# Performance work log

Measured on AMD Instinct MI355X. Metric: run time of the kernel, lower is better.

## Reference

```python
import jax, jax.numpy as jnp
import numpy as np

DIM = 1024
NUM_HEADS = 16
HEAD_DIM = DIM // NUM_HEADS
MLP_RATIO = 4
NUM_EXPERTS = 4
B, N = 4, 1024


def _ln(x, g, b, eps=1e-5):
    m = jnp.mean(x, axis=-1, keepdims=True)
    v = jnp.mean(jnp.square(x - m), axis=-1, keepdims=True)
    return (x - m) * jax.lax.rsqrt(v + eps) * g + b


def setup_inputs() -> dict:
    key = jax.random.key(0)
    ks = jax.random.split(key, 8)
    d = DIM
    return {
        "x": jax.random.normal(ks[0], (B, N, d), jnp.float32),
        "expert_mask": jax.random.randint(ks[1], (B, N), 0, NUM_EXPERTS),
        "expert_probs": jax.random.uniform(ks[2], (B, N, 1), jnp.float32),
        "expand_weight": 0.02 * jax.random.normal(ks[3], (3 * d + MLP_RATIO * d, d), jnp.float32),
        "mlp_bias": 0.02 * jax.random.normal(ks[4], (MLP_RATIO * d,), jnp.float32),
        "contract_weight": 0.02 * jax.random.normal(ks[5], (2 * d, d + MLP_RATIO * d), jnp.float32),
        "contract_bias": 0.02 * jax.random.normal(ks[6], (2 * d,), jnp.float32),
        "norm1_g": jnp.ones((d,), jnp.float32),
        "norm1_b": jnp.zeros((d,), jnp.float32),
        "norm2_g": jnp.ones((d,), jnp.float32),
        "norm2_b": jnp.zeros((d,), jnp.float32),
        "alpha": 0.1 * jax.random.normal(ks[7], (1,), jnp.float32),
    }


def reference(x, expert_mask, expert_probs, expand_weight, mlp_bias, contract_weight,
              contract_bias, norm1_g, norm1_b, norm2_g, norm2_b, alpha):
    Bx, Nx, D = x.shape
    # nested capacity per token: D_e = D // 2**(E-1-e)
    d_e = D // jnp.power(2, NUM_EXPERTS - 1 - expert_mask)          # [B,N] int
    fmask = (jnp.arange(D) < d_e[..., None]).astype(x.dtype)        # [B,N,D]

    residual = x
    # bias as in source: concat([mlp_bias, zeros(3d)]) added to full expand output
    input_bias = jnp.concatenate([mlp_bias, jnp.zeros((3 * D,), x.dtype)], axis=-1)

    # nested_linear_expand: token uses only first D_e input features
    xn = _ln(x, norm1_g, norm1_b) * fmask
    y = jnp.einsum('bnd,ed->bne', xn, expand_weight) + input_bias   # [B,N,7D]

    qkv = y[..., : 3 * D]
    mlp_hidden = y[..., 3 * D:] + mlp_bias                          # [B,N,4D]

    q = qkv[..., :D]
    k = _ln(qkv[..., D:2 * D], norm2_g, norm2_b)
    v = _ln(qkv[..., 2 * D:], norm2_g, norm2_b)

    def heads(t):
        return t.reshape(Bx, Nx, NUM_HEADS, HEAD_DIM).transpose(0, 2, 1, 3)

    scale = HEAD_DIM ** -0.5
    attn = jax.nn.softmax(jnp.einsum('bhqd,bhkd->bhqk', heads(q) * scale, heads(k)), axis=-1)
    attn_out = jnp.einsum('bhqk,bhkd->bhqd', attn, heads(v)).transpose(0, 2, 1, 3).reshape(Bx, Nx, D)

    h = jnp.concatenate([attn_out, jax.nn.gelu(mlp_hidden, approximate=False)], axis=-1)  # [B,N,5D]
    # nested_linear_contract: only first D_e outputs per D-sized half are produced
    out = jnp.einsum('bnf,of->bno', h, contract_weight) + contract_bias                   # [B,N,2D]
    out = out * jnp.concatenate([fmask, fmask], axis=-1)

    attn_branch = out[..., :D] + residual
    return attn_branch + (alpha * expert_probs + 1.0) * out[..., D:]
```

## Files before the change

### kernel.cpp

```cpp
#include <hip/hip_runtime.h>
#include <hip/hip_bf16.h>

typedef __attribute__((ext_vector_type(8))) short bf16x8;
typedef __attribute__((ext_vector_type(4))) short s16x4;
typedef __attribute__((ext_vector_type(4))) float f32x4;

#define DIM    1024
#define TOKENS 4096
#define NHEAD  16
#define HD     64
#define EXP_N  7168
#define CON_N  2048
#define HF     5120

#define WEXP_OFF 0u
#define XN_OFF   14680064u
#define WC_OFF   0u
#define Q_OFF    23068672u
#define K_OFF    31457280u
#define V_OFF    39845888u
#define H_OFF    48234496u
#define PERM_OFF 90177536u
#define DSRT_OFF 90193920u
#define TMAX_OFF 90210304u
#define OUT2_OFF 23068672u

__device__ __forceinline__ short f2bf(float f) {
  union { __hip_bfloat16 h; short s; } u;
  u.h = __float2bfloat16(f);
  return u.s;
}
__device__ __forceinline__ float bf2f(short s) {
  unsigned int u = ((unsigned int)(unsigned short)s) << 16;
  return __builtin_bit_cast(float, u);
}

__device__ __forceinline__ void gload16(const void* g, void* l) {
  __builtin_amdgcn_global_load_lds((const __attribute__((address_space(1))) void*)g,
                                   (__attribute__((address_space(3))) void*)l,
                                   16, 0, 0);
}

__device__ __forceinline__ void block_reduce_2(float& a, float& b) {
  #pragma unroll
  for (int off = 32; off > 0; off >>= 1) {
    a += __shfl_down(a, off);
    b += __shfl_down(b, off);
  }
  __shared__ float red[2][4];
  int wid = threadIdx.x >> 6, lane = threadIdx.x & 63;
  if (lane == 0) { red[0][wid] = a; red[1][wid] = b; }
  __syncthreads();
  a = red[0][0] + red[0][1] + red[0][2] + red[0][3];
  b = red[1][0] + red[1][1] + red[1][2] + red[1][3];
}

__global__ __launch_bounds__(256) void sort_kernel(const int* __restrict__ emask,
                                                   int* __restrict__ perm,
                                                   int* __restrict__ de_sorted,
                                                   int* __restrict__ tile_demax) {
  __shared__ int cnt[4][256];
  __shared__ int boff[4];
  __shared__ int lm[256];
  const int t = threadIdx.x;
  const int lane = t & 63, w = t >> 6;
  int msk[16];
  int lc4[4] = {0, 0, 0, 0};
  #pragma unroll
  for (int j = 0; j < 16; ++j) { msk[j] = emask[t * 16 + j]; lc4[msk[j]]++; }
  #pragma unroll
  for (int b = 0; b < 4; ++b) cnt[b][t] = lc4[b];
  __syncthreads();
  {
    int v0 = cnt[w][lane * 4], v1 = cnt[w][lane * 4 + 1];
    int v2 = cnt[w][lane * 4 + 2], v3 = cnt[w][lane * 4 + 3];
    int s = v0 + v1 + v2 + v3;
    int inc = s;
    #pragma unroll
    for (int off = 1; off < 64; off <<= 1) {
      int n = __shfl_up(inc, off);
      if (lane >= off) inc += n;
    }
    int ex = inc - s;
    cnt[w][lane * 4]     = ex;
    cnt[w][lane * 4 + 1] = ex + v0;
    cnt[w][lane * 4 + 2] = ex + v0 + v1;
    cnt[w][lane * 4 + 3] = ex + v0 + v1 + v2;
    if (lane == 63) boff[w] = inc;
  }
  __syncthreads();
  if (t == 0) {
    int t0 = boff[0], t1 = boff[1], t2 = boff[2];
    boff[0] = 0; boff[1] = t0; boff[2] = t0 + t1; boff[3] = t0 + t1 + t2;
  }
  __syncthreads();
  int c4[4] = {0, 0, 0, 0};
  #pragma unroll
  for (int j = 0; j < 16; ++j) {
    int b = msk[j];
    int pos = boff[b] + cnt[b][t] + c4[b]++;
    perm[pos] = t * 16 + j;
    de_sorted[pos] = DIM >> (3 - b);
  }
  __syncthreads();
  int mx = 0;
  #pragma unroll
  for (int j = 0; j < 16; ++j) mx = max(mx, de_sorted[t * 16 + j]);
  lm[t] = mx;
  __syncthreads();
  if (t < 32) {
    int m2 = 0;
    #pragma unroll
    for (int j = 0; j < 8; ++j) m2 = max(m2, lm[t * 8 + j]);
    tile_demax[t] = m2;
  }
}

__global__ __launch_bounds__(256) void f2bf_kernel(const float* __restrict__ in,
                                                   short* __restrict__ outp, int n4) {
  for (int i = blockIdx.x * blockDim.x + threadIdx.x; i < n4; i += gridDim.x * blockDim.x) {
    f32x4 xv = *(const f32x4*)(&in[(size_t)i * 4]);
    s16x4 o = { f2bf(xv[0]), f2bf(xv[1]), f2bf(xv[2]), f2bf(xv[3]) };
    *(s16x4*)(&outp[(size_t)i * 4]) = o;
  }
}

__global__ __launch_bounds__(256) void ln1_kernel(const float* __restrict__ x,
                                                  const int* __restrict__ emask,
                                                  const float* __restrict__ g,
                                                  const float* __restrict__ bb,
                                                  short* __restrict__ xn) {
  int m = blockIdx.x, t = threadIdx.x;
  const float* row = x + (size_t)m * DIM;
  f32x4 xv = *(const f32x4*)(&row[t * 4]);
  float s  = xv[0] + xv[1] + xv[2] + xv[3];
  float ss = xv[0] * xv[0] + xv[1] * xv[1] + xv[2] * xv[2] + xv[3] * xv[3];
  block_reduce_2(s, ss);
  float mean = s * (1.0f / DIM);
  float var  = ss * (1.0f / DIM) - mean * mean;
  float inv  = rsqrtf(var + 1e-5f);
  int de = DIM >> (3 - emask[m]);
  s16x4 o;
  #pragma unroll
  for (int jj = 0; jj < 4; ++jj) {
    int c = t * 4 + jj;
    float v = (c < de) ? ((xv[jj] - mean) * inv * g[c] + bb[c]) : 0.f;
    o[jj] = f2bf(v);
  }
  *(s16x4*)(&xn[(size_t)m * DIM + t * 4]) = o;
}

#define STAGE(Asb, Bsb, kk)                                   \
  do {                                                        \
    gload16(Ap0 + (kk), (Asb) + ch0 * 512);                   \
    gload16(Ap1 + (kk), (Asb) + ch1 * 512);                   \
    gload16(Bp0 + (kk), (Bsb) + ch0 * 512);                   \
    gload16(Bp1 + (kk), (Bsb) + ch1 * 512);                   \
  } while (0)

#define COMPUTE(Asb, Bsb)                                                     \
  do {                                                                        \
    bf16x8 af[4], bfr[4];                                                     \
    _Pragma("unroll")                                                         \
    for (int i = 0; i < 4; ++i)                                               \
      af[i] = *(const bf16x8*)(&(Asb)[(wr * 64 + i * 16 + lc) * 32 + lg * 8]);\
    _Pragma("unroll")                                                         \
    for (int j = 0; j < 4; ++j)                                               \
      bfr[j] = *(const bf16x8*)(&(Bsb)[(wc * 64 + j * 16 + lc) * 32 + lg * 8]);\
    _Pragma("unroll")                                                         \
    for (int i = 0; i < 4; ++i)                                               \
      _Pragma("unroll")                                                       \
      for (int j = 0; j < 4; ++j)                                             \
        acc[i][j] = __builtin_amdgcn_mfma_f32_16x16x32_bf16(af[i], bfr[j],    \
                                                            acc[i][j], 0, 0, 0);\
  } while (0)

__device__ __forceinline__ void gemm_core_128(const short* __restrict__ A,
                                              const short* __restrict__ B,
                                              int lda, int ldb, int K,
                                              int m0, int n0,
                                              const int* __restrict__ aperm,
                                              short* As0, short* As1,
                                              short* Bs0, short* Bs1,
                                              f32x4 acc[4][4]) {
  const int tid = threadIdx.x;
  const int lane = tid & 63;
  const int wid = tid >> 6;
  const int wr = wid >> 1, wc = wid & 1;
  const int lg = lane >> 4, lc = lane & 15;
  const int r4 = lane >> 2;
  const int c8 = (lane & 3) * 8;
  const int ch0 = wid * 2, ch1 = wid * 2 + 1;
  int ra0 = m0 + ch0 * 16 + r4, ra1 = m0 + ch1 * 16 + r4;
  if (aperm) { ra0 = aperm[ra0]; ra1 = aperm[ra1]; }
  const short* Ap0 = A + (size_t)ra0 * lda + c8;
  const short* Ap1 = A + (size_t)ra1 * lda + c8;
  const short* Bp0 = B + (size_t)(n0 + ch0 * 16 + r4) * ldb + c8;
  const short* Bp1 = B + (size_t)(n0 + ch1 * 16 + r4) * ldb + c8;

  STAGE(As0, Bs0, 0);
  for (int k0 = 0; k0 < K; k0 += 64) {
    __syncthreads();
    STAGE(As1, Bs1, k0 + 32);
    COMPUTE(As0, Bs0);
    __syncthreads();
    if (k0 + 64 < K) STAGE(As0, Bs0, k0 + 64);
    COMPUTE(As1, Bs1);
  }
}

__device__ __forceinline__ void xcd_swizzle_cm(int& bx, int& by) {
  int nwg = gridDim.x * gridDim.y;
  int bid = blockIdx.y * gridDim.x + blockIdx.x;
  int cpx = nwg >> 3;
  int swz = (bid & 7) * cpx + (bid >> 3);
  by = swz % gridDim.y;
  bx = swz / gridDim.y;
}

__global__ __launch_bounds__(256) void gemm1_kernel(const short* __restrict__ xn,
                                                    const short* __restrict__ Wexp,
                                                    const float* __restrict__ mlpb,
                                                    const int* __restrict__ perm,
                                                    const int* __restrict__ tmax,
                                                    short* __restrict__ qbuf,
                                                    short* __restrict__ kbuf,
                                                    short* __restrict__ vbuf,
                                                    short* __restrict__ hbuf) {
  __shared__ __align__(16) short As0[128 * 32], As1[128 * 32];
  __shared__ __align__(16) short Bs0[128 * 32], Bs1[128 * 32];
  f32x4 acc[4][4];
  f32x4 z = {0.f, 0.f, 0.f, 0.f};
  #pragma unroll
  for (int i = 0; i < 4; ++i)
    #pragma unroll
    for (int j = 0; j < 4; ++j) acc[i][j] = z;
  int bx, by;
  xcd_swizzle_cm(bx, by);
  int n0 = bx * 128;
  int m0 = by * 128;
  int kmax = tmax[by];
  gemm_core_128(xn, Wexp, DIM, DIM, kmax, m0, n0, perm, As0, As1, Bs0, Bs1, acc);
  const int tid = threadIdx.x, lane = tid & 63, wid = tid >> 6;
  const int wr = wid >> 1, wc = wid & 1, lg = lane >> 4, lc = lane & 15;
  int toks[4][4];
  #pragma unroll
  for (int i = 0; i < 4; ++i)
    #pragma unroll
    for (int r = 0; r < 4; ++r)
      toks[i][r] = perm[m0 + wr * 64 + i * 16 + lg * 4 + r];
  #pragma unroll
  for (int i = 0; i < 4; ++i) {
    #pragma unroll
    for (int j = 0; j < 4; ++j) {
      int e = n0 + wc * 64 + j * 16 + lc;
      #pragma unroll
      for (int r = 0; r < 4; ++r) {
        int m = toks[i][r];
        float val = acc[i][j][r];
        if (e < DIM) {
          qbuf[(size_t)m * DIM + e] = f2bf((val + mlpb[e]) * 0.125f);
        } else if (e < 2 * DIM) {
          kbuf[(size_t)m * DIM + (e - DIM)] = f2bf(val + mlpb[e]);
        } else if (e < 3 * DIM) {
          vbuf[(size_t)m * DIM + (e - 2 * DIM)] = f2bf(val + mlpb[e]);
        } else {
          int jj = e - 3 * DIM;
          float xx = val + mlpb[jj] + (e < 4 * DIM ? mlpb[e] : 0.f);
          float ge = 0.5f * xx * (1.f + erff(xx * 0.70710678118654752f));
          hbuf[(size_t)m * HF + DIM + jj] = f2bf(ge);
        }
      }
    }
  }
}

__global__ __launch_bounds__(256) void ln2_kernel(short* __restrict__ kbuf,
                                                  short* __restrict__ vbuf,
                                                  const float* __restrict__ g,
                                                  const float* __restrict__ bb) {
  int rr = blockIdx.x;
  int m = rr >> 1;
  short* row = ((rr & 1) ? vbuf : kbuf) + (size_t)m * DIM;
  int t = threadIdx.x;
  s16x4 iv = *(const s16x4*)(&row[t * 4]);
  float f[4];
  #pragma unroll
  for (int jj = 0; jj < 4; ++jj) f[jj] = bf2f(iv[jj]);
  float s = f[0] + f[1] + f[2] + f[3];
  float ss = f[0] * f[0] + f[1] * f[1] + f[2] * f[2] + f[3] * f[3];
  block_reduce_2(s, ss);
  float mean = s * (1.0f / DIM);
  float var  = ss * (1.0f / DIM) - mean * mean;
  float inv  = rsqrtf(var + 1e-5f);
  s16x4 o;
  #pragma unroll
  for (int jj = 0; jj < 4; ++jj) {
    int c = t * 4 + jj;
    o[jj] = f2bf((f[jj] - mean) * inv * g[c] + bb[c]);
  }
  *(s16x4*)(&row[t * 4]) = o;
}

__global__ __launch_bounds__(256) void attn_kernel(const short* __restrict__ q,
                                                   const short* __restrict__ k,
                                                   const short* __restrict__ v,
                                                   short* __restrict__ hbuf) {
  __shared__ __align__(16) short Kt[64 * 72];
  __shared__ __align__(16) short Vt[64 * 72];
  __shared__ __align__(16) short Pl[4][16 * 72];
  const int bh = blockIdx.x;
  const int b = bh >> 4, hh = bh & 15;
  const int qt = blockIdx.y;
  const int tid = threadIdx.x, w = tid >> 6, lane = tid & 63;
  const int lg = lane >> 4, lc = lane & 15;

  bf16x8 qa0, qa1;
  {
    const short* qbase = q + ((size_t)(b * 1024 + qt * 64 + w * 16 + lc)) * DIM + hh * HD;
    qa0 = *(const bf16x8*)(qbase + lg * 8);
    qa1 = *(const bf16x8*)(qbase + 32 + lg * 8);
  }
  f32x4 po[4];
  f32x4 z = {0.f, 0.f, 0.f, 0.f};
  #pragma unroll
  for (int d = 0; d < 4; ++d) po[d] = z;
  float mrun[4] = {-INFINITY, -INFINITY, -INFINITY, -INFINITY};
  float lsum[4] = {0.f, 0.f, 0.f, 0.f};

  for (int kt = 0; kt < 16; ++kt) {
    __syncthreads();
    const int kc0 = kt * 64;
    #pragma unroll
    for (int it = 0; it < 2; ++it) {
      int row = (tid >> 3) + it * 32;
      int c8 = (tid & 7) * 8;
      size_t gb = ((size_t)(b * 1024 + kc0 + row)) * DIM + hh * HD + c8;
      *(bf16x8*)(&Kt[row * 72 + c8]) = *(const bf16x8*)(&k[gb]);
      bf16x8 vv = *(const bf16x8*)(&v[gb]);
      #pragma unroll
      for (int jj = 0; jj < 8; ++jj) Vt[(c8 + jj) * 72 + row] = vv[jj];
    }
    __syncthreads();
    f32x4 sacc[4];
    #pragma unroll
    for (int cb = 0; cb < 4; ++cb) {
      bf16x8 kb0 = *(const bf16x8*)(&Kt[(cb * 16 + lc) * 72 + lg * 8]);
      bf16x8 kb1 = *(const bf16x8*)(&Kt[(cb * 16 + lc) * 72 + 32 + lg * 8]);
      f32x4 t0 = __builtin_amdgcn_mfma_f32_16x16x32_bf16(qa0, kb0, z, 0, 0, 0);
      sacc[cb] = __builtin_amdgcn_mfma_f32_16x16x32_bf16(qa1, kb1, t0, 0, 0, 0);
    }
    #pragma unroll
    for (int r = 0; r < 4; ++r) {
      float mx = fmaxf(fmaxf(sacc[0][r], sacc[1][r]), fmaxf(sacc[2][r], sacc[3][r]));
      #pragma unroll
      for (int off = 1; off < 16; off <<= 1) mx = fmaxf(mx, __shfl_xor(mx, off));
      float mnew = fmaxf(mrun[r], mx);
      float al = __expf(mrun[r] - mnew);
      mrun[r] = mnew;
      float ps = 0.f;
      #pragma unroll
      for (int cb = 0; cb < 4; ++cb) {
        float p = __expf(sacc[cb][r] - mnew);
        sacc[cb][r] = p;
        ps += p;
      }
      #pragma unroll
      for (int off = 1; off < 16; off <<= 1) ps += __shfl_xor(ps, off);
      lsum[r] = lsum[r] * al + ps;
      #pragma unroll
      for (int d = 0; d < 4; ++d) po[d][r] *= al;
    }
    #pragma unroll
    for (int cb = 0; cb < 4; ++cb)
      #pragma unroll
      for (int r = 0; r < 4; ++r)
        Pl[w][(lg * 4 + r) * 72 + cb * 16 + lc] = f2bf(sacc[cb][r]);
    __syncthreads();
    bf16x8 pa0 = *(const bf16x8*)(&Pl[w][lc * 72 + lg * 8]);
    bf16x8 pa1 = *(const bf16x8*)(&Pl[w][lc * 72 + 32 + lg * 8]);
    #pragma unroll
    for (int d = 0; d < 4; ++d) {
      bf16x8 vb0 = *(const bf16x8*)(&Vt[(d * 16 + lc) * 72 + lg * 8]);
      bf16x8 vb1 = *(const bf16x8*)(&Vt[(d * 16 + lc) * 72 + 32 + lg * 8]);
      po[d] = __builtin_amdgcn_mfma_f32_16x16x32_bf16(pa0, vb0, po[d], 0, 0, 0);
      po[d] = __builtin_amdgcn_mfma_f32_16x16x32_bf16(pa1, vb1, po[d], 0, 0, 0);
    }
  }
  #pragma unroll
  for (int d = 0; d < 4; ++d)
    #pragma unroll
    for (int r = 0; r < 4; ++r) {
      int token = b * 1024 + qt * 64 + w * 16 + lg * 4 + r;
      float o = po[d][r] / lsum[r];
      hbuf[(size_t)token * HF + hh * HD + d * 16 + lc] = f2bf(o);
    }
}

__global__ __launch_bounds__(256) void gemm2_kernel(const short* __restrict__ h,
                                                    const short* __restrict__ Wc,
                                                    const float* __restrict__ cbias,
                                                    const int* __restrict__ perm,
                                                    const int* __restrict__ dsrt,
                                                    const int* __restrict__ tmax,
                                                    short* __restrict__ out2) {
  __shared__ __align__(16) short As0[128 * 32], As1[128 * 32];
  __shared__ __align__(16) short Bs0[128 * 32], Bs1[128 * 32];
  f32x4 acc[4][4];
  f32x4 z = {0.f, 0.f, 0.f, 0.f};
  #pragma unroll
  for (int i = 0; i < 4; ++i)
    #pragma unroll
    for (int j = 0; j < 4; ++j) acc[i][j] = z;
  int bx, by;
  xcd_swizzle_cm(bx, by);
  int n0 = bx * 128;
  int m0 = by * 128;
  int demax = tmax[by];
  if ((n0 & (DIM - 1)) < demax)
    gemm_core_128(h, Wc, HF, HF, HF, m0, n0, perm, As0, As1, Bs0, Bs1, acc);
  const int tid = threadIdx.x, lane = tid & 63, wid = tid >> 6;
  const int wr = wid >> 1, wc = wid & 1, lg = lane >> 4, lc = lane & 15;
  int toks[4][4], des[4][4];
  #pragma unroll
  for (int i = 0; i < 4; ++i)
    #pragma unroll
    for (int r = 0; r < 4; ++r) {
      int ms = m0 + wr * 64 + i * 16 + lg * 4 + r;
      toks[i][r] = perm[ms];
      des[i][r] = dsrt[ms];
    }
  #pragma unroll
  for (int i = 0; i < 4; ++i) {
    #pragma unroll
    for (int j = 0; j < 4; ++j) {
      int o = n0 + wc * 64 + j * 16 + lc;
      float bias = cbias[o];
      #pragma unroll
      for (int r = 0; r < 4; ++r) {
        float val = acc[i][j][r] + bias;
        if ((o & (DIM - 1)) >= des[i][r]) val = 0.f;
        out2[(size_t)toks[i][r] * CON_N + o] = f2bf(val);
      }
    }
  }
}

__global__ __launch_bounds__(256) void combine_kernel(const float* __restrict__ x,
                                                      const float* __restrict__ probs,
                                                      const float* __restrict__ alpha,
                                                      const short* __restrict__ out2,
                                                      float* __restrict__ out) {
  int m = blockIdx.x, t = threadIdx.x;
  float coef = alpha[0] * probs[m] + 1.0f;
  f32x4 xv = *(const f32x4*)(&x[(size_t)m * DIM + t * 4]);
  s16x4 o1 = *(const s16x4*)(&out2[(size_t)m * CON_N + t * 4]);
  s16x4 o2 = *(const s16x4*)(&out2[(size_t)m * CON_N + DIM + t * 4]);
  f32x4 r;
  #pragma unroll
  for (int jj = 0; jj < 4; ++jj) r[jj] = xv[jj] + bf2f(o1[jj]) + coef * bf2f(o2[jj]);
  *(f32x4*)(&out[(size_t)m * DIM + t * 4]) = r;
}

extern "C" void kernel_launch(void* const* d_in, const int* in_sizes, int n_in,
                              void* d_out, int out_size, void* d_ws, size_t ws_size,
                              hipStream_t stream) {
  (void)in_sizes; (void)n_in; (void)out_size; (void)ws_size;
  const float* x     = (const float*)d_in[0];
  const int*   emask = (const int*)d_in[1];
  const float* probs = (const float*)d_in[2];
  const float* Wexp  = (const float*)d_in[3];
  const float* mlpb  = (const float*)d_in[4];
  const float* Wc    = (const float*)d_in[5];
  const float* cbias = (const float*)d_in[6];
  const float* n1g   = (const float*)d_in[7];
  const float* n1b   = (const float*)d_in[8];
  const float* n2g   = (const float*)d_in[9];
  const float* n2b   = (const float*)d_in[10];
  const float* alpha = (const float*)d_in[11];
  float* out = (float*)d_out;
  char* ws = (char*)d_ws;

  short* wexp_bf = (short*)(ws + WEXP_OFF);
  short* xn      = (short*)(ws + XN_OFF);
  short* wc_bf   = (short*)(ws + WC_OFF);
  short* qbuf    = (short*)(ws + Q_OFF);
  short* kbuf    = (short*)(ws + K_OFF);
  short* vbuf    = (short*)(ws + V_OFF);
  short* hbuf    = (short*)(ws + H_OFF);
  short* out2    = (short*)(ws + OUT2_OFF);
  int*   perm    = (int*)(ws + PERM_OFF);
  int*   dsrt    = (int*)(ws + DSRT_OFF);
  int*   tmaxb   = (int*)(ws + TMAX_OFF);

  hipLaunchKernelGGL(sort_kernel, dim3(1), dim3(256), 0, stream, emask, perm, dsrt, tmaxb);
  hipLaunchKernelGGL(f2bf_kernel, dim3(2048), dim3(256), 0, stream, Wexp, wexp_bf, (EXP_N * DIM) / 4);
  hipLaunchKernelGGL(ln1_kernel, dim3(TOKENS), dim3(256), 0, stream, x, emask, n1g, n1b, xn);
  hipLaunchKernelGGL(gemm1_kernel, dim3(EXP_N / 128, TOKENS / 128), dim3(256), 0, stream,
                     xn, wexp_bf, mlpb, perm, tmaxb, qbuf, kbuf, vbuf, hbuf);
  hipLaunchKernelGGL(f2bf_kernel, dim3(2048), dim3(256), 0, stream, Wc, wc_bf, (CON_N * HF) / 4);
  hipLaunchKernelGGL(ln2_kernel, dim3(2 * TOKENS), dim3(256), 0, stream, kbuf, vbuf, n2g, n2b);
  hipLaunchKernelGGL(attn_kernel, dim3(64, 16), dim3(256), 0, stream, qbuf, kbuf, vbuf, hbuf);
  hipLaunchKernelGGL(gemm2_kernel, dim3(CON_N / 128, TOKENS / 128), dim3(256), 0, stream,
                     hbuf, wc_bf, cbias, perm, dsrt, tmaxb, out2);
  hipLaunchKernelGGL(combine_kernel, dim3(TOKENS), dim3(256), 0, stream, x, probs, alpha, out2, out);
}
```

Measured before the change: 350.8 us.

## Triple-buffer GEMM shared-memory staging with explicit vmcnt waits

After: 344.1 us. Within noise of the previous version (-1.9%).

```diff
diff --git a/kernel.cpp b/kernel.cpp
--- a/kernel.cpp
+++ b/kernel.cpp
@@ -150,6 +150,8 @@
   *(s16x4*)(&xn[(size_t)m * DIM + t * 4]) = o;
 }
 
+#define GBUF 4096
+
 #define STAGE(Asb, Bsb, kk)                                   \
   do {                                                        \
     gload16(Ap0 + (kk), (Asb) + ch0 * 512);                   \
@@ -175,13 +177,14 @@
                                                             acc[i][j], 0, 0, 0);\
   } while (0)
 
+#define VMCNT(n) asm volatile("s_waitcnt vmcnt(" #n ")" ::: "memory")
+
 __device__ __forceinline__ void gemm_core_128(const short* __restrict__ A,
                                               const short* __restrict__ B,
                                               int lda, int ldb, int K,
                                               int m0, int n0,
                                               const int* __restrict__ aperm,
-                                              short* As0, short* As1,
-                                              short* Bs0, short* Bs1,
+                                              short* AS, short* BS,
                                               f32x4 acc[4][4]) {
   const int tid = threadIdx.x;
   const int lane = tid & 63;
@@ -198,14 +201,35 @@
   const short* Bp0 = B + (size_t)(n0 + ch0 * 16 + r4) * ldb + c8;
   const short* Bp1 = B + (size_t)(n0 + ch1 * 16 + r4) * ldb + c8;
 
-  STAGE(As0, Bs0, 0);
-  for (int k0 = 0; k0 < K; k0 += 64) {
-    __syncthreads();
-    STAGE(As1, Bs1, k0 + 32);
-    COMPUTE(As0, Bs0);
-    __syncthreads();
-    if (k0 + 64 < K) STAGE(As0, Bs0, k0 + 64);
-    COMPUTE(As1, Bs1);
+  const int nt = K >> 5;
+  STAGE(AS + 0 * GBUF, BS + 0 * GBUF, 0);
+  STAGE(AS + 1 * GBUF, BS + 1 * GBUF, 32);
+  STAGE(AS + 2 * GBUF, BS + 2 * GBUF, 64);
+  int cur = 0;
+  for (int t = 0; t < nt - 2; ++t) {
+    short* Ac = AS + cur * GBUF;
+    short* Bc = BS + cur * GBUF;
+    VMCNT(8);
+    __builtin_amdgcn_s_barrier();
+    COMPUTE(Ac, Bc);
+    __builtin_amdgcn_s_barrier();
+    if (t < nt - 3) STAGE(Ac, Bc, (t + 3) * 32);
+    cur = (cur == 2) ? 0 : cur + 1;
+  }
+  {
+    short* Ac = AS + cur * GBUF;
+    short* Bc = BS + cur * GBUF;
+    VMCNT(4);
+    __builtin_amdgcn_s_barrier();
+    COMPUTE(Ac, Bc);
+    cur = (cur == 2) ? 0 : cur + 1;
+  }
+  {
+    short* Ac = AS + cur * GBUF;
+    short* Bc = BS + cur * GBUF;
+    VMCNT(0);
+    __builtin_amdgcn_s_barrier();
+    COMPUTE(Ac, Bc);
   }
 }
 
@@ -227,8 +251,8 @@
                                                     short* __restrict__ kbuf,
                                                     short* __restrict__ vbuf,
                                                     short* __restrict__ hbuf) {
-  __shared__ __align__(16) short As0[128 * 32], As1[128 * 32];
-  __shared__ __align__(16) short Bs0[128 * 32], Bs1[128 * 32];
+  __shared__ __align__(16) short AS[3 * GBUF];
+  __shared__ __align__(16) short BS[3 * GBUF];
   f32x4 acc[4][4];
   f32x4 z = {0.f, 0.f, 0.f, 0.f};
   #pragma unroll
@@ -240,7 +264,7 @@
   int n0 = bx * 128;
   int m0 = by * 128;
   int kmax = tmax[by];
-  gemm_core_128(xn, Wexp, DIM, DIM, kmax, m0, n0, perm, As0, As1, Bs0, Bs1, acc);
+  gemm_core_128(xn, Wexp, DIM, DIM, kmax, m0, n0, perm, AS, BS, acc);
   const int tid = threadIdx.x, lane = tid & 63, wid = tid >> 6;
   const int wr = wid >> 1, wc = wid & 1, lg = lane >> 4, lc = lane & 15;
   int toks[4][4];
@@ -404,8 +428,8 @@
                                                     const int* __restrict__ dsrt,
                                                     const int* __restrict__ tmax,
                                                     short* __restrict__ out2) {
-  __shared__ __align__(16) short As0[128 * 32], As1[128 * 32];
-  __shared__ __align__(16) short Bs0[128 * 32], Bs1[128 * 32];
+  __shared__ __align__(16) short AS[3 * GBUF];
+  __shared__ __align__(16) short BS[3 * GBUF];
   f32x4 acc[4][4];
   f32x4 z = {0.f, 0.f, 0.f, 0.f};
   #pragma unroll
@@ -418,7 +442,7 @@
   int m0 = by * 128;
   int demax = tmax[by];
   if ((n0 & (DIM - 1)) < demax)
-    gemm_core_128(h, Wc, HF, HF, HF, m0, n0, perm, As0, As1, Bs0, Bs1, acc);
+    gemm_core_128(h, Wc, HF, HF, HF, m0, n0, perm, AS, BS, acc);
   const int tid = threadIdx.x, lane = tid & 63, wid = tid >> 6;
   const int wr = wid >> 1, wc = wid & 1, lg = lane >> 4, lc = lane & 15;
   int toks[4][4], des[4][4];
```
